# Optimization experiments

Measured on AMD Instinct MI355X. Metric: run time of the kernel, lower is better.

## Reference

```python
import jax, jax.numpy as jnp
import numpy as np
import math

D_MODEL = 1024
EXPAND = 2
D_INNER = EXPAND * D_MODEL        # 2048
HEADDIM = 64
NHEADS = D_INNER // HEADDIM       # 32
D_STATE = 128
D_CONV = 4
CHUNK = 128
SEQLEN = 4096
BATCH = 1                         # bidirectional merge in forward hard-codes batch=1
CONV_DIM = D_INNER + 2 * (2 * D_STATE)            # 2560
D_IN_PROJ = 2 * D_INNER + 2 * (2 * D_STATE) + 2 * NHEADS  # 4672
EPS = 1e-5


def silu(x):
    return x * jax.nn.sigmoid(x)


def segsum_exp(a):
    """exp(segsum(a)): out[..., i, j] = exp(sum_{k=j+1..i} a[..., k]) for i>=j else 0."""
    T = a.shape[-1]
    m1 = jnp.tril(jnp.ones((T, T), bool), -1)
    s = jnp.cumsum(jnp.where(m1, a[..., :, None], 0.0), axis=-2)
    m0 = jnp.tril(jnp.ones((T, T), bool))
    return jnp.where(m0, jnp.exp(jnp.where(m0, s, 0.0)), 0.0)


def ssd(x, A, B, C, chunk):
    """x:(b,L,h,p) A:(b,L,h) B,C:(b,L,n) (head dim of size 1 squeezed). L % chunk == 0."""
    b, L, h, p = x.shape
    c = L // chunk
    x = x.reshape(b, c, chunk, h, p)
    A = A.reshape(b, c, chunk, h).transpose(0, 3, 1, 2)   # (b,h,c,l)
    B = B.reshape(b, c, chunk, -1)
    C = C.reshape(b, c, chunk, -1)
    A_cs = jnp.cumsum(A, axis=-1)                          # (b,h,c,l)
    Lmat = segsum_exp(A)                                   # (b,h,c,l,l)
    # intra-chunk (diagonal block) outputs
    Y_diag = jnp.einsum('bcln,bcsn,bhcls,bcshp->bclhp', C, B, Lmat, x)
    # per-chunk states
    decay_states = jnp.exp(A_cs[..., -1:] - A_cs)          # (b,h,c,l)
    states = jnp.einsum('bcln,bhcl,bclhp->bchpn', B, decay_states, x)
    states = jnp.concatenate([jnp.zeros_like(states[:, :1]), states], axis=1)
    # inter-chunk recurrence via segsum over chunk boundaries
    decay_chunk = segsum_exp(jnp.pad(A_cs[..., -1], ((0, 0), (0, 0), (1, 0))))  # (b,h,c+1,c+1)
    new_states = jnp.einsum('bhzc,bchpn->bzhpn', decay_chunk, states)
    states, final_state = new_states[:, :-1], new_states[:, -1]
    Y_off = jnp.einsum('bcln,bchpn,bhcl->bclhp', C, states, jnp.exp(A_cs))
    Y = (Y_diag + Y_off).reshape(b, L, h, p)
    return Y, final_state


def setup_inputs() -> dict:
    key = jax.random.key(0)
    ks = jax.random.split(key, 8)
    s = 0.02
    u = jax.random.normal(ks[0], (BATCH, SEQLEN, D_MODEL), jnp.float32)
    in_proj_w = jax.random.normal(ks[1], (D_IN_PROJ, D_MODEL), jnp.float32) * s
    conv_w = jax.random.normal(ks[2], (CONV_DIM, 1, D_CONV), jnp.float32) * (1.0 / math.sqrt(D_CONV))
    conv_b = jnp.zeros((CONV_DIM,), jnp.float32)
    dt = jnp.exp(jax.random.uniform(ks[3], (NHEADS,)) * (math.log(0.1) - math.log(0.001)) + math.log(0.001))
    dt = jnp.clip(dt, 1e-4)
    dt_bias = dt + jnp.log(-jnp.expm1(-dt))
    A_log = jnp.log(jax.random.uniform(ks[4], (NHEADS,), minval=1.0, maxval=16.0))
    D = jnp.ones((NHEADS,), jnp.float32)
    fc_D_w = jax.random.normal(ks[5], (NHEADS, D_INNER), jnp.float32) * s
    norm_w = jnp.ones((D_INNER,), jnp.float32)
    out_proj_w = jax.random.normal(ks[6], (D_MODEL, D_INNER), jnp.float32) * s
    return dict(u=u, in_proj_w=in_proj_w, conv_w=conv_w, conv_b=conv_b, dt_bias=dt_bias,
                A_log=A_log, D=D, fc_D_w=fc_D_w, norm_w=norm_w, out_proj_w=out_proj_w)


def reference(u, in_proj_w, conv_w, conv_b, dt_bias, A_log, D, fc_D_w, norm_w, out_proj_w):
    b, l, _ = u.shape
    zxbcdt = u @ in_proj_w.T                               # (b,l,D_IN_PROJ)
    z = zxbcdt[..., :D_INNER]
    xBC = zxbcdt[..., D_INNER:D_INNER + CONV_DIM]
    dt = zxbcdt[..., D_INNER + CONV_DIM:]                  # (b,l,2*nheads)
    # fwd heads + time-reversed bwd heads stacked on batch dim
    dt = jnp.concatenate([dt[..., :NHEADS], jnp.flip(dt[..., NHEADS:], axis=1)], axis=0)
    dt = jax.nn.softplus(dt + dt_bias)                     # (2b,l,nheads)
    # depthwise causal conv1d + silu
    xc = jnp.transpose(xBC, (0, 2, 1))                     # (b,CONV_DIM,l)
    xc = jax.lax.conv_general_dilated(xc, conv_w, (1,), [(D_CONV - 1, 0)],
                                      feature_group_count=CONV_DIM,
                                      dimension_numbers=('NCH', 'OIH', 'NCH'))
    xc = xc + conv_b[None, :, None]
    xBC = silu(jnp.transpose(xc, (0, 2, 1)))               # (b,l,CONV_DIM)
    x = xBC[..., :D_INNER]
    BC = xBC[..., D_INNER:]
    x_og = x
    x2 = jnp.concatenate([x, jnp.flip(x, 1)], axis=0)      # (2b,l,d_inner)
    BC = jnp.concatenate([BC[..., :2 * D_STATE], jnp.flip(BC[..., 2 * D_STATE:], 1)], axis=0)
    B = BC[..., :D_STATE]
    C = BC[..., D_STATE:]
    xh = x2.reshape(2 * b, l, NHEADS, HEADDIM)
    A = -jnp.exp(A_log)
    Y, final_state = ssd(xh * dt[..., None], A * dt, B, C, CHUNK)
    y = Y + xh * D[:, None]
    y = y.reshape(2 * b, l, D_INNER)
    # torch.roll(shift=1, dim=1) then zero first step == shift right with zero pad
    y = jnp.concatenate([jnp.zeros_like(y[:, :1]), y[:, :-1]], axis=1)
    y_fw, y_bw = y[:b], jnp.flip(y[b:], 1)
    fd = x_og @ fc_D_w.T + D                               # F.linear(x_og, fc_D.weight, bias=D)
    y = y_fw + y_bw + x_og * jnp.repeat(fd, HEADDIM, axis=-1)
    # gated RMSNorm
    yg = y * silu(z)
    yn = yg * jax.lax.rsqrt(jnp.mean(yg * yg, axis=-1, keepdims=True) + EPS) * norm_w
    return yn @ out_proj_w.T
```

## Files before the change

### kernel.cpp

```cpp
#include <hip/hip_runtime.h>
#include <hip/hip_bf16.h>
#include <math.h>

#define L_SEQ   4096
#define DMODEL  1024
#define DINNER  2048
#define NHEADS  32
#define HEADDIM 64
#define DSTATE  128
#define NCHUNK  32
#define CHUNKL  128
#define CONVDIM 2560
#define DPROJ   4672
#define NPAD1   4736

typedef __hip_bfloat16 bf16;
__device__ __forceinline__ float b2f(bf16 x) { return __bfloat162float(x); }
__device__ __forceinline__ bf16 f2b(float x) { return __float2bfloat16(x); }
__device__ __forceinline__ float sh2f(short s) {
  return __uint_as_float(((unsigned int)(unsigned short)s) << 16);
}
__device__ __forceinline__ short f2bs(float x) {
  bf16 t = __float2bfloat16(x);
  return *reinterpret_cast<short*>(&t);
}

typedef __attribute__((ext_vector_type(8))) short bf16x8v;
typedef __attribute__((ext_vector_type(4))) float f32x4v;

__device__ __forceinline__ float dot8(bf16x8v x, float4 w0, float4 w1) {
  return sh2f(x[0]) * w0.x + sh2f(x[1]) * w0.y + sh2f(x[2]) * w0.z + sh2f(x[3]) * w0.w +
         sh2f(x[4]) * w1.x + sh2f(x[5]) * w1.y + sh2f(x[6]) * w1.z + sh2f(x[7]) * w1.w;
}


__global__ __launch_bounds__(256) void cast_kernel(
    const float* __restrict__ src, bf16* __restrict__ dst, int n_src, int n_tot) {
  int i = blockIdx.x * 256 + threadIdx.x;
  if (i < n_tot) dst[i] = (i < n_src) ? f2b(src[i]) : f2b(0.f);
}

template <typename TC>
__global__ __launch_bounds__(256) void gemm_mfma(
    const bf16* __restrict__ A, int lda,
    const bf16* __restrict__ B, int ldb,
    TC* __restrict__ C, int ldc,
    int N, int K, int gridM) {
  __shared__ short As[128][32];
  __shared__ short Bs[128][32];
  int tid = threadIdx.x;
  int lane = tid & 63;
  int w = tid >> 6;
  int wr = w >> 1, wc = w & 1;
  int bid = blockIdx.x;
  int mst = gridM >> 3;
  int xk = bid & 7, q = bid >> 3;
  int bm = (xk + 8 * (q % mst)) * 128;
  int bn = (q / mst) * 128;
  f32x4v acc[4][4];
#pragma unroll
  for (int i = 0; i < 4; i++)
#pragma unroll
    for (int j = 0; j < 4; j++) acc[i][j] = (f32x4v){0.f, 0.f, 0.f, 0.f};

  const bf16* Ab = A + (size_t)(bm + w * 32 + (lane >> 2)) * lda + (lane & 3) * 8;
  const bf16* Bb = B + (size_t)(bn + w * 32 + (lane >> 2)) * ldb + (lane & 3) * 8;

  for (int k0 = 0; k0 < K; k0 += 32) {
    __builtin_amdgcn_global_load_lds(
        (const __attribute__((address_space(1))) void*)(Ab + k0),
        (__attribute__((address_space(3))) void*)&As[w * 32][0], 16, 0, 0);
    __builtin_amdgcn_global_load_lds(
        (const __attribute__((address_space(1))) void*)(Ab + (size_t)16 * lda + k0),
        (__attribute__((address_space(3))) void*)&As[w * 32 + 16][0], 16, 0, 0);
    __builtin_amdgcn_global_load_lds(
        (const __attribute__((address_space(1))) void*)(Bb + k0),
        (__attribute__((address_space(3))) void*)&Bs[w * 32][0], 16, 0, 0);
    __builtin_amdgcn_global_load_lds(
        (const __attribute__((address_space(1))) void*)(Bb + (size_t)16 * ldb + k0),
        (__attribute__((address_space(3))) void*)&Bs[w * 32 + 16][0], 16, 0, 0);
    __syncthreads();
    bf16x8v af[4], bv[4];
#pragma unroll
    for (int i = 0; i < 4; i++)
      af[i] = *(const bf16x8v*)&As[wr * 64 + i * 16 + (lane & 15)][(lane >> 4) * 8];
#pragma unroll
    for (int j = 0; j < 4; j++)
      bv[j] = *(const bf16x8v*)&Bs[wc * 64 + j * 16 + (lane & 15)][(lane >> 4) * 8];
#pragma unroll
    for (int i = 0; i < 4; i++)
#pragma unroll
      for (int j = 0; j < 4; j++)
        acc[i][j] = __builtin_amdgcn_mfma_f32_16x16x32_bf16(af[i], bv[j], acc[i][j], 0, 0, 0);
    __syncthreads();
  }
  int quad = lane >> 4;
  int cn = lane & 15;
#pragma unroll
  for (int i = 0; i < 4; i++) {
#pragma unroll
    for (int j = 0; j < 4; j++) {
      int col = bn + wc * 64 + j * 16 + cn;
      if (col < N) {
#pragma unroll
        for (int r = 0; r < 4; r++) {
          int row = bm + wr * 64 + i * 16 + quad * 4 + r;
          float v = acc[i][j][r];
          if constexpr (sizeof(TC) == 2) C[(size_t)row * ldc + col] = f2b(v);
          else                           C[(size_t)row * ldc + col] = v;
        }
      }
    }
  }
}

__global__ __launch_bounds__(256) void fc_kernel(
    const bf16* __restrict__ xbc, const float* __restrict__ Wf,
    const float* __restrict__ Dp, float* __restrict__ fd) {
  int lane = threadIdx.x & 63;
  int w = threadIdx.x >> 6;
  int t0 = (blockIdx.x * 4 + w) * 4;
  int h = lane & 31;
  int g = lane >> 5;
  const float* wr = Wf + (size_t)h * DINNER + g * 1024;
  const bf16* xr = xbc + (size_t)t0 * CONVDIM + g * 1024;
  float a0 = 0.f, a1 = 0.f, a2 = 0.f, a3 = 0.f;
  for (int k = 0; k < 1024; k += 8) {
    float4 w0 = *(const float4*)(wr + k);
    float4 w1 = *(const float4*)(wr + k + 4);
    bf16x8v x0 = *(const bf16x8v*)(xr + k);
    bf16x8v x1 = *(const bf16x8v*)(xr + CONVDIM + k);
    bf16x8v x2 = *(const bf16x8v*)(xr + 2 * CONVDIM + k);
    bf16x8v x3 = *(const bf16x8v*)(xr + 3 * CONVDIM + k);
    a0 += dot8(x0, w0, w1);
    a1 += dot8(x1, w0, w1);
    a2 += dot8(x2, w0, w1);
    a3 += dot8(x3, w0, w1);
  }
  a0 += __shfl_down(a0, 32);
  a1 += __shfl_down(a1, 32);
  a2 += __shfl_down(a2, 32);
  a3 += __shfl_down(a3, 32);
  if (lane < 32) {
    float d = Dp[h];
    fd[(t0 + 0) * NHEADS + h] = a0 + d;
    fd[(t0 + 1) * NHEADS + h] = a1 + d;
    fd[(t0 + 2) * NHEADS + h] = a2 + d;
    fd[(t0 + 3) * NHEADS + h] = a3 + d;
  }
}

__global__ __launch_bounds__(256) void conv_silu_kernel(
    const bf16* __restrict__ zx, const float* __restrict__ conv_w,
    const float* __restrict__ conv_b, bf16* __restrict__ xbc) {
  int idx = blockIdx.x * 256 + threadIdx.x;
  if (idx >= (L_SEQ / 4) * CONVDIM) return;
  int ch = idx % CONVDIM;
  int t0 = (idx / CONVDIM) * 4;
  const bf16* col = zx + DINNER + ch;
  float w0 = conv_w[ch * 4 + 0], w1 = conv_w[ch * 4 + 1];
  float w2 = conv_w[ch * 4 + 2], w3 = conv_w[ch * 4 + 3];
  float bsv = conv_b[ch];
  float x[7];
#pragma unroll
  for (int i = 0; i < 7; i++) {
    int t = t0 - 3 + i;
    x[i] = (t >= 0) ? b2f(col[(size_t)t * DPROJ]) : 0.f;
  }
#pragma unroll
  for (int j = 0; j < 4; j++) {
    float acc = bsv + w0 * x[j] + w1 * x[j + 1] + w2 * x[j + 2] + w3 * x[j + 3];
    xbc[(size_t)(t0 + j) * CONVDIM + ch] = f2b(acc / (1.f + __expf(-acc)));
  }
}

__global__ __launch_bounds__(256) void dt_kernel(
    const bf16* __restrict__ zx, const float* __restrict__ dt_bias,
    float* __restrict__ dt2) {
  int idx = blockIdx.x * 256 + threadIdx.x;
  if (idx >= 2 * L_SEQ * NHEADS) return;
  int h = idx % NHEADS;
  int t = (idx / NHEADS) % L_SEQ;
  int b = idx / (NHEADS * L_SEQ);
  float v;
  if (b == 0) v = b2f(zx[(size_t)t * DPROJ + 4608 + h]);
  else        v = b2f(zx[(size_t)(L_SEQ - 1 - t) * DPROJ + 4608 + NHEADS + h]);
  v += dt_bias[h];
  dt2[idx] = (v > 20.f) ? v : log1pf(expf(v));
}

__global__ __launch_bounds__(256) void gmat_kernel(
    const bf16* __restrict__ xbc, bf16* __restrict__ G) {
  __shared__ bf16 Cs[128][136];
  __shared__ bf16 Bs[128][136];
  int bc = blockIdx.x;
  int b = bc / NCHUNK, c = bc % NCHUNK;
  int tid = threadIdx.x;
  int lane = tid & 63;
  int w = tid >> 6;
  int bofs = b ? 2304 : 2048;
  int cofs = b ? 2432 : 2176;
  for (int o = tid; o < CHUNKL * DSTATE / 8; o += 256) {
    int s = o >> 4;
    int n8 = (o & 15) * 8;
    int t = b ? (L_SEQ - 1 - (c * CHUNKL + s)) : (c * CHUNKL + s);
    const bf16* row = xbc + (size_t)t * CONVDIM;
    *(bf16x8v*)&Bs[s][n8] = *(const bf16x8v*)&row[bofs + n8];
    *(bf16x8v*)&Cs[s][n8] = *(const bf16x8v*)&row[cofs + n8];
  }
  __syncthreads();
  f32x4v acc[2][8];
#pragma unroll
  for (int i = 0; i < 2; i++)
#pragma unroll
    for (int j = 0; j < 8; j++) acc[i][j] = (f32x4v){0.f, 0.f, 0.f, 0.f};
#pragma unroll
  for (int k0 = 0; k0 < 128; k0 += 32) {
    bf16x8v a0 = *(const bf16x8v*)&Cs[w * 32 + (lane & 15)][(lane >> 4) * 8 + k0];
    bf16x8v a1 = *(const bf16x8v*)&Cs[w * 32 + 16 + (lane & 15)][(lane >> 4) * 8 + k0];
#pragma unroll
    for (int j = 0; j < 8; j++) {
      bf16x8v bv = *(const bf16x8v*)&Bs[j * 16 + (lane & 15)][(lane >> 4) * 8 + k0];
      acc[0][j] = __builtin_amdgcn_mfma_f32_16x16x32_bf16(a0, bv, acc[0][j], 0, 0, 0);
      acc[1][j] = __builtin_amdgcn_mfma_f32_16x16x32_bf16(a1, bv, acc[1][j], 0, 0, 0);
    }
  }
  int quad = lane >> 4, cn = lane & 15;
  bf16* Gb = G + (size_t)bc * CHUNKL * CHUNKL;
#pragma unroll
  for (int i = 0; i < 2; i++)
#pragma unroll
    for (int j = 0; j < 8; j++)
#pragma unroll
      for (int r = 0; r < 4; r++) {
        int l = w * 32 + i * 16 + quad * 4 + r;
        int s = j * 16 + cn;
        Gb[l * CHUNKL + s] = f2b(acc[i][j][r]);
      }
}

__global__ __launch_bounds__(256) void chunk_kernel(
    const bf16* __restrict__ xbc, const float* __restrict__ dt2,
    const float* __restrict__ A_log,
    bf16* __restrict__ states, float* __restrict__ csum) {
  int gid = blockIdx.x;
  int h = gid % NHEADS;
  int bc = gid / NHEADS;
  int c = bc % NCHUNK, b = bc / NCHUNK;
  int tid = threadIdx.x;
  int lane = tid & 63;
  int w = tid >> 6;
  __shared__ bf16 BdT[128][136];
  __shared__ bf16 xdtT[64][136];
  __shared__ float acs[CHUNKL];
  __shared__ float dtl[CHUNKL];
  __shared__ float decays[CHUNKL];
  if (tid < CHUNKL)
    dtl[tid] = dt2[((size_t)b * L_SEQ + c * CHUNKL + tid) * NHEADS + h];
  __syncthreads();
  if (tid == 0) {
    float Ah = -__expf(A_log[h]);
    float s = 0.f;
    for (int l = 0; l < CHUNKL; l++) { s += Ah * dtl[l]; acs[l] = s; }
    csum[gid] = __expf(s);
  }
  __syncthreads();
  if (tid < CHUNKL) decays[tid] = __expf(acs[CHUNKL - 1] - acs[tid]);
  for (int o = tid; o < CHUNKL * HEADDIM / 8; o += 256) {
    int s = o & 127;
    int p8 = (o >> 7) * 8;
    int t = b ? (L_SEQ - 1 - (c * CHUNKL + s)) : (c * CHUNKL + s);
    bf16x8v xv = *(const bf16x8v*)&xbc[(size_t)t * CONVDIM + h * HEADDIM + p8];
    float d = dtl[s];
#pragma unroll
    for (int j = 0; j < 8; j++) xdtT[p8 + j][s] = f2b(sh2f(xv[j]) * d);
  }
  __syncthreads();
  for (int o = tid; o < CHUNKL * CHUNKL / 8; o += 256) {
    int l = o & 127;
    int n8 = (o >> 7) * 8;
    int t = b ? (L_SEQ - 1 - (c * CHUNKL + l)) : (c * CHUNKL + l);
    bf16x8v bv = *(const bf16x8v*)&xbc[(size_t)t * CONVDIM + (b ? 2304 : 2048) + n8];
    float d = decays[l];
#pragma unroll
    for (int j = 0; j < 8; j++) BdT[n8 + j][l] = f2b(sh2f(bv[j]) * d);
  }
  __syncthreads();
  f32x4v accS[8];
#pragma unroll
  for (int j = 0; j < 8; j++) accS[j] = (f32x4v){0.f, 0.f, 0.f, 0.f};
#pragma unroll
  for (int k0 = 0; k0 < 128; k0 += 32) {
    bf16x8v av = *(const bf16x8v*)&xdtT[w * 16 + (lane & 15)][(lane >> 4) * 8 + k0];
#pragma unroll
    for (int j = 0; j < 8; j++) {
      bf16x8v bv = *(const bf16x8v*)&BdT[j * 16 + (lane & 15)][(lane >> 4) * 8 + k0];
      accS[j] = __builtin_amdgcn_mfma_f32_16x16x32_bf16(av, bv, accS[j], 0, 0, 0);
    }
  }
  int quad = lane >> 4, cn = lane & 15;
  bf16* st = states + (size_t)gid * (HEADDIM * DSTATE);
#pragma unroll
  for (int j = 0; j < 8; j++)
#pragma unroll
    for (int r = 0; r < 4; r++) {
      int p = w * 16 + quad * 4 + r;
      int n = j * 16 + cn;
      st[p * DSTATE + n] = f2b(accS[j][r]);
    }
}

__global__ __launch_bounds__(256) void scan_kernel(
    bf16* __restrict__ states, const float* __restrict__ csum) {
  int idx = blockIdx.x * 256 + threadIdx.x;
  int n = idx % DSTATE;
  int p = (idx / DSTATE) % HEADDIM;
  int h = (idx / (DSTATE * HEADDIM)) % NHEADS;
  int b = idx / (DSTATE * HEADDIM * NHEADS);
  float S = 0.f;
  for (int c = 0; c < NCHUNK; c++) {
    int gid = (b * NCHUNK + c) * NHEADS + h;
    size_t off = (size_t)gid * (HEADDIM * DSTATE) + p * DSTATE + n;
    float tmp = b2f(states[off]);
    states[off] = f2b(S);
    S = csum[gid] * S + tmp;
  }
}

__global__ __launch_bounds__(256) void yoff_kernel(
    const bf16* __restrict__ xbc, const float* __restrict__ dt2,
    const float* __restrict__ A_log, const bf16* __restrict__ G,
    const bf16* __restrict__ states, const float* __restrict__ Dp,
    bf16* __restrict__ Y) {
  int gid = blockIdx.x;
  int h = gid % NHEADS;
  int bc = gid / NHEADS;
  int c = bc % NCHUNK, b = bc / NCHUNK;
  int tid = threadIdx.x;
  int lane = tid & 63;
  int w = tid >> 6;
  __shared__ bf16 WB[128][136];
  __shared__ bf16 SX[64][136];
  __shared__ float acs[CHUNKL];
  __shared__ float dtl[CHUNKL];
  __shared__ float eAl[CHUNKL];
  if (tid < CHUNKL)
    dtl[tid] = dt2[((size_t)b * L_SEQ + c * CHUNKL + tid) * NHEADS + h];
  __syncthreads();
  if (tid == 0) {
    float Ah = -__expf(A_log[h]);
    float s = 0.f;
    for (int l = 0; l < CHUNKL; l++) { s += Ah * dtl[l]; acs[l] = s; }
  }
  __syncthreads();
  if (tid < CHUNKL) eAl[tid] = __expf(acs[tid]);
  for (int o = tid; o < CHUNKL * HEADDIM / 8; o += 256) {
    int s = o & 127;
    int p8 = (o >> 7) * 8;
    int t = b ? (L_SEQ - 1 - (c * CHUNKL + s)) : (c * CHUNKL + s);
    bf16x8v xv = *(const bf16x8v*)&xbc[(size_t)t * CONVDIM + h * HEADDIM + p8];
    float d = dtl[s];
#pragma unroll
    for (int j = 0; j < 8; j++) SX[p8 + j][s] = f2b(sh2f(xv[j]) * d);
  }
  {
    const bf16* Gb = G + (size_t)bc * CHUNKL * CHUNKL;
    for (int o = tid; o < CHUNKL * CHUNKL / 8; o += 256) {
      int l = o >> 4;
      int s8 = (o & 15) * 8;
      bf16x8v g = *(const bf16x8v*)&Gb[l * CHUNKL + s8];
      float al = acs[l];
      bf16x8v wv;
#pragma unroll
      for (int j = 0; j < 8; j++) {
        int s = s8 + j;
        float e = (s <= l) ? sh2f(g[j]) * __expf(al - acs[s]) : 0.f;
        wv[j] = f2bs(e);
      }
      *(bf16x8v*)&WB[l][s8] = wv;
    }
  }
  __syncthreads();
  f32x4v accY[2][4];
#pragma unroll
  for (int i = 0; i < 2; i++)
#pragma unroll
    for (int j = 0; j < 4; j++) accY[i][j] = (f32x4v){0.f, 0.f, 0.f, 0.f};
#pragma unroll
  for (int k0 = 0; k0 < 128; k0 += 32) {
    bf16x8v a0 = *(const bf16x8v*)&WB[w * 32 + (lane & 15)][(lane >> 4) * 8 + k0];
    bf16x8v a1 = *(const bf16x8v*)&WB[w * 32 + 16 + (lane & 15)][(lane >> 4) * 8 + k0];
#pragma unroll
    for (int j = 0; j < 4; j++) {
      bf16x8v bv = *(const bf16x8v*)&SX[j * 16 + (lane & 15)][(lane >> 4) * 8 + k0];
      accY[0][j] = __builtin_amdgcn_mfma_f32_16x16x32_bf16(a0, bv, accY[0][j], 0, 0, 0);
      accY[1][j] = __builtin_amdgcn_mfma_f32_16x16x32_bf16(a1, bv, accY[1][j], 0, 0, 0);
    }
  }
  __syncthreads();
  {
    int cofs = b ? 2432 : 2176;
    for (int o = tid; o < CHUNKL * DSTATE / 8; o += 256) {
      int l = o >> 4;
      int n8 = (o & 15) * 8;
      int t = b ? (L_SEQ - 1 - (c * CHUNKL + l)) : (c * CHUNKL + l);
      bf16x8v cv = *(const bf16x8v*)&xbc[(size_t)t * CONVDIM + cofs + n8];
      float e = eAl[l];
      bf16x8v ov;
#pragma unroll
      for (int j = 0; j < 8; j++) ov[j] = f2bs(sh2f(cv[j]) * e);
      *(bf16x8v*)&WB[l][n8] = ov;
    }
    const bf16* stp = states + (size_t)gid * (HEADDIM * DSTATE);
    for (int o = tid; o < HEADDIM * DSTATE / 8; o += 256) {
      int p = o >> 4;
      int n8 = (o & 15) * 8;
      *(bf16x8v*)&SX[p][n8] = *(const bf16x8v*)&stp[o * 8];
    }
  }
  __syncthreads();
#pragma unroll
  for (int k0 = 0; k0 < 128; k0 += 32) {
    bf16x8v a0 = *(const bf16x8v*)&WB[w * 32 + (lane & 15)][(lane >> 4) * 8 + k0];
    bf16x8v a1 = *(const bf16x8v*)&WB[w * 32 + 16 + (lane & 15)][(lane >> 4) * 8 + k0];
#pragma unroll
    for (int j = 0; j < 4; j++) {
      bf16x8v bv = *(const bf16x8v*)&SX[j * 16 + (lane & 15)][(lane >> 4) * 8 + k0];
      accY[0][j] = __builtin_amdgcn_mfma_f32_16x16x32_bf16(a0, bv, accY[0][j], 0, 0, 0);
      accY[1][j] = __builtin_amdgcn_mfma_f32_16x16x32_bf16(a1, bv, accY[1][j], 0, 0, 0);
    }
  }
  int quad = lane >> 4, cn = lane & 15;
  float Dh = Dp[h];
#pragma unroll
  for (int i = 0; i < 2; i++)
#pragma unroll
    for (int j = 0; j < 4; j++)
#pragma unroll
      for (int r = 0; r < 4; r++) {
        int l = w * 32 + i * 16 + quad * 4 + r;
        int p = j * 16 + cn;
        int t = b ? (L_SEQ - 1 - (c * CHUNKL + l)) : (c * CHUNKL + l);
        float xv = b2f(xbc[(size_t)t * CONVDIM + h * HEADDIM + p]);
        size_t yi = ((size_t)b * L_SEQ + c * CHUNKL + l) * DINNER + h * HEADDIM + p;
        Y[yi] = f2b(accY[i][j][r] + xv * Dh);
      }
}

__global__ __launch_bounds__(256) void combine_kernel(
    const bf16* __restrict__ Y, const bf16* __restrict__ xbc,
    const bf16* __restrict__ zx, const float* __restrict__ fd,
    const float* __restrict__ norm_w, bf16* __restrict__ yn) {
  int t = blockIdx.x;
  int tid = threadIdx.x;
  int j8 = tid * 8;
  float yf[8], yb[8];
#pragma unroll
  for (int j = 0; j < 8; j++) { yf[j] = 0.f; yb[j] = 0.f; }
  if (t >= 1) {
    bf16x8v v = *(const bf16x8v*)&Y[(size_t)(t - 1) * DINNER + j8];
#pragma unroll
    for (int j = 0; j < 8; j++) yf[j] = sh2f(v[j]);
  }
  if (t <= L_SEQ - 2) {
    bf16x8v v = *(const bf16x8v*)&Y[((size_t)L_SEQ + (L_SEQ - 2 - t)) * DINNER + j8];
#pragma unroll
    for (int j = 0; j < 8; j++) yb[j] = sh2f(v[j]);
  }
  bf16x8v xogv = *(const bf16x8v*)&xbc[(size_t)t * CONVDIM + j8];
  bf16x8v zv = *(const bf16x8v*)&zx[(size_t)t * DPROJ + j8];
  float fdv = fd[t * NHEADS + (j8 >> 6)];
  float yg[8];
  float ss = 0.f;
#pragma unroll
  for (int j = 0; j < 8; j++) {
    float y = yf[j] + yb[j] + sh2f(xogv[j]) * fdv;
    float z = sh2f(zv[j]);
    float g = y * (z / (1.f + __expf(-z)));
    yg[j] = g;
    ss += g * g;
  }
#pragma unroll
  for (int off = 32; off > 0; off >>= 1) ss += __shfl_down(ss, off);
  __shared__ float red[4];
  if ((tid & 63) == 0) red[tid >> 6] = ss;
  __syncthreads();
  float tot = red[0] + red[1] + red[2] + red[3];
  float scale = rsqrtf(tot / (float)DINNER + 1e-5f);
  float4 nw0 = *(const float4*)&norm_w[j8];
  float4 nw1 = *(const float4*)&norm_w[j8 + 4];
  bf16x8v ov;
  ov[0] = f2bs(yg[0] * scale * nw0.x);
  ov[1] = f2bs(yg[1] * scale * nw0.y);
  ov[2] = f2bs(yg[2] * scale * nw0.z);
  ov[3] = f2bs(yg[3] * scale * nw0.w);
  ov[4] = f2bs(yg[4] * scale * nw1.x);
  ov[5] = f2bs(yg[5] * scale * nw1.y);
  ov[6] = f2bs(yg[6] * scale * nw1.z);
  ov[7] = f2bs(yg[7] * scale * nw1.w);
  *(bf16x8v*)&yn[(size_t)t * DINNER + j8] = ov;
}

extern "C" void kernel_launch(void* const* d_in, const int* in_sizes, int n_in,
                              void* d_out, int out_size, void* d_ws, size_t ws_size,
                              hipStream_t stream) {
  const float* u         = (const float*)d_in[0];
  const float* in_proj_w = (const float*)d_in[1];
  const float* conv_w    = (const float*)d_in[2];
  const float* conv_b    = (const float*)d_in[3];
  const float* dt_bias   = (const float*)d_in[4];
  const float* A_log     = (const float*)d_in[5];
  const float* Dp        = (const float*)d_in[6];
  const float* fc_D_w    = (const float*)d_in[7];
  const float* norm_w    = (const float*)d_in[8];
  const float* out_proj_w= (const float*)d_in[9];
  float* out = (float*)d_out;

  char* base = (char*)d_ws;
  bf16*  zx  = (bf16*)base;  base += (size_t)L_SEQ * DPROJ * 2;
  bf16*  xbc = (bf16*)base;  base += (size_t)L_SEQ * CONVDIM * 2;
  float* dt2 = (float*)base; base += (size_t)2 * L_SEQ * NHEADS * 4;
  bf16*  G   = (bf16*)base;  base += (size_t)2 * NCHUNK * CHUNKL * CHUNKL * 4;
  bf16*  Yb  = (bf16*)base;  base += (size_t)2 * L_SEQ * DINNER * 4;
  bf16*  stb = (bf16*)base;  base += (size_t)2 * NCHUNK * NHEADS * HEADDIM * DSTATE * 4;
  float* cs  = (float*)base; base += (size_t)2 * NCHUNK * NHEADS * 4;
  bf16*  u_bf   = (bf16*)Yb;
  bf16*  w1p_bf = (bf16*)((char*)Yb + 9437184);
  bf16*  w2_bf  = (bf16*)G;
  bf16*  yn     = (bf16*)stb;
  float* fd     = (float*)((char*)stb + 33554432);

  cast_kernel<<<(L_SEQ * DMODEL + 255) / 256, 256, 0, stream>>>(
      u, u_bf, L_SEQ * DMODEL, L_SEQ * DMODEL);
  cast_kernel<<<(NPAD1 * DMODEL + 255) / 256, 256, 0, stream>>>(
      in_proj_w, w1p_bf, DPROJ * DMODEL, NPAD1 * DMODEL);
  gemm_mfma<bf16><<<(L_SEQ / 128) * (NPAD1 / 128), 256, 0, stream>>>(
      u_bf, DMODEL, w1p_bf, DMODEL, zx, DPROJ, DPROJ, DMODEL, L_SEQ / 128);
  conv_silu_kernel<<<((L_SEQ / 4) * CONVDIM + 255) / 256, 256, 0, stream>>>(
      zx, conv_w, conv_b, xbc);
  dt_kernel<<<(2 * L_SEQ * NHEADS + 255) / 256, 256, 0, stream>>>(
      zx, dt_bias, dt2);
  gmat_kernel<<<2 * NCHUNK, 256, 0, stream>>>(xbc, G);
  chunk_kernel<<<2 * NCHUNK * NHEADS, 256, 0, stream>>>(
      xbc, dt2, A_log, stb, cs);
  scan_kernel<<<(2 * NHEADS * HEADDIM * DSTATE) / 256, 256, 0, stream>>>(stb, cs);
  yoff_kernel<<<2 * NCHUNK * NHEADS, 256, 0, stream>>>(
      xbc, dt2, A_log, G, stb, Dp, Yb);
  cast_kernel<<<(DMODEL * DINNER + 255) / 256, 256, 0, stream>>>(
      out_proj_w, w2_bf, DMODEL * DINNER, DMODEL * DINNER);
  fc_kernel<<<L_SEQ / 16, 256, 0, stream>>>(xbc, fc_D_w, Dp, fd);
  combine_kernel<<<L_SEQ, 256, 0, stream>>>(Yb, xbc, zx, fd, norm_w, yn);
  gemm_mfma<float><<<(L_SEQ / 128) * (DMODEL / 128), 256, 0, stream>>>(
      yn, DINNER, w2_bf, DINNER, out, DMODEL, DMODEL, DINNER, L_SEQ / 128);
}
```

Baseline: 413.5 us.

## Merge cast and conv/dt launches, split gmat into quarters, preload scan chunks

Merges the two input casts into one launch and the conv/SiLU and dt kernels into one launch, which removes launch overhead. Splits gmat into four blocks per chunk so it runs on 256 blocks instead of 64, and each block computes only the lower-triangular tiles its warp needs. The scan kernel now loads all chunk states and decay factors up front, so the loads no longer sit on the serial dependency chain. The first GEMM drops its block swizzle for row-major block order, which may change L2 reuse.

```diff
diff --git a/kernel.cpp b/kernel.cpp
--- a/kernel.cpp
+++ b/kernel.cpp
@@ -34,6 +34,20 @@
 }
 
 
+__global__ __launch_bounds__(256) void cast2_kernel(
+    const float* __restrict__ u, const float* __restrict__ w1,
+    bf16* __restrict__ u_bf, bf16* __restrict__ w1_bf) {
+  const int NU = (L_SEQ * DMODEL) / 256;
+  int bid = blockIdx.x;
+  if (bid < NU) {
+    int i = bid * 256 + threadIdx.x;
+    u_bf[i] = f2b(u[i]);
+  } else {
+    int i = (bid - NU) * 256 + threadIdx.x;
+    w1_bf[i] = (i < DPROJ * DMODEL) ? f2b(w1[i]) : f2b(0.f);
+  }
+}
+
 __global__ __launch_bounds__(256) void cast_kernel(
     const float* __restrict__ src, bf16* __restrict__ dst, int n_src, int n_tot) {
   int i = blockIdx.x * 256 + threadIdx.x;
@@ -45,7 +59,7 @@
     const bf16* __restrict__ A, int lda,
     const bf16* __restrict__ B, int ldb,
     TC* __restrict__ C, int ldc,
-    int N, int K, int gridM) {
+    int N, int K, int gridM, int gridN, int swz) {
   __shared__ short As[128][32];
   __shared__ short Bs[128][32];
   int tid = threadIdx.x;
@@ -53,10 +67,16 @@
   int w = tid >> 6;
   int wr = w >> 1, wc = w & 1;
   int bid = blockIdx.x;
-  int mst = gridM >> 3;
-  int xk = bid & 7, q = bid >> 3;
-  int bm = (xk + 8 * (q % mst)) * 128;
-  int bn = (q / mst) * 128;
+  int bm, bn;
+  if (swz) {
+    int mst = gridM >> 3;
+    int xk = bid & 7, q = bid >> 3;
+    bm = (xk + 8 * (q % mst)) * 128;
+    bn = (q / mst) * 128;
+  } else {
+    bm = (bid / gridN) * 128;
+    bn = (bid % gridN) * 128;
+  }
   f32x4v acc[4][4];
 #pragma unroll
   for (int i = 0; i < 4; i++)
@@ -150,51 +170,53 @@
   }
 }
 
-__global__ __launch_bounds__(256) void conv_silu_kernel(
+#define CONV_BLOCKS ((L_SEQ / 4) * CONVDIM / 256)
+__global__ __launch_bounds__(256) void conv_dt_kernel(
     const bf16* __restrict__ zx, const float* __restrict__ conv_w,
-    const float* __restrict__ conv_b, bf16* __restrict__ xbc) {
-  int idx = blockIdx.x * 256 + threadIdx.x;
-  if (idx >= (L_SEQ / 4) * CONVDIM) return;
-  int ch = idx % CONVDIM;
-  int t0 = (idx / CONVDIM) * 4;
-  const bf16* col = zx + DINNER + ch;
-  float w0 = conv_w[ch * 4 + 0], w1 = conv_w[ch * 4 + 1];
-  float w2 = conv_w[ch * 4 + 2], w3 = conv_w[ch * 4 + 3];
-  float bsv = conv_b[ch];
-  float x[7];
-#pragma unroll
-  for (int i = 0; i < 7; i++) {
-    int t = t0 - 3 + i;
-    x[i] = (t >= 0) ? b2f(col[(size_t)t * DPROJ]) : 0.f;
-  }
-#pragma unroll
-  for (int j = 0; j < 4; j++) {
-    float acc = bsv + w0 * x[j] + w1 * x[j + 1] + w2 * x[j + 2] + w3 * x[j + 3];
-    xbc[(size_t)(t0 + j) * CONVDIM + ch] = f2b(acc / (1.f + __expf(-acc)));
-  }
-}
-
-__global__ __launch_bounds__(256) void dt_kernel(
-    const bf16* __restrict__ zx, const float* __restrict__ dt_bias,
-    float* __restrict__ dt2) {
-  int idx = blockIdx.x * 256 + threadIdx.x;
-  if (idx >= 2 * L_SEQ * NHEADS) return;
-  int h = idx % NHEADS;
-  int t = (idx / NHEADS) % L_SEQ;
-  int b = idx / (NHEADS * L_SEQ);
-  float v;
-  if (b == 0) v = b2f(zx[(size_t)t * DPROJ + 4608 + h]);
-  else        v = b2f(zx[(size_t)(L_SEQ - 1 - t) * DPROJ + 4608 + NHEADS + h]);
-  v += dt_bias[h];
-  dt2[idx] = (v > 20.f) ? v : log1pf(expf(v));
+    const float* __restrict__ conv_b, bf16* __restrict__ xbc,
+    const float* __restrict__ dt_bias, float* __restrict__ dt2) {
+  int bid = blockIdx.x;
+  if (bid < CONV_BLOCKS) {
+    int idx = bid * 256 + threadIdx.x;
+    int ch = idx % CONVDIM;
+    int t0 = (idx / CONVDIM) * 4;
+    const bf16* col = zx + DINNER + ch;
+    float w0 = conv_w[ch * 4 + 0], w1 = conv_w[ch * 4 + 1];
+    float w2 = conv_w[ch * 4 + 2], w3 = conv_w[ch * 4 + 3];
+    float bsv = conv_b[ch];
+    float x[7];
+#pragma unroll
+    for (int i = 0; i < 7; i++) {
+      int t = t0 - 3 + i;
+      x[i] = (t >= 0) ? b2f(col[(size_t)t * DPROJ]) : 0.f;
+    }
+#pragma unroll
+    for (int j = 0; j < 4; j++) {
+      float acc = bsv + w0 * x[j] + w1 * x[j + 1] + w2 * x[j + 2] + w3 * x[j + 3];
+      xbc[(size_t)(t0 + j) * CONVDIM + ch] = f2b(acc / (1.f + __expf(-acc)));
+    }
+  } else {
+    int idx = (bid - CONV_BLOCKS) * 256 + threadIdx.x;
+    int h = idx % NHEADS;
+    int t = (idx / NHEADS) % L_SEQ;
+    int b = idx / (NHEADS * L_SEQ);
+    float v;
+    if (b == 0) v = b2f(zx[(size_t)t * DPROJ + 4608 + h]);
+    else        v = b2f(zx[(size_t)(L_SEQ - 1 - t) * DPROJ + 4608 + NHEADS + h]);
+    v += dt_bias[h];
+    dt2[idx] = (v > 20.f) ? v : log1pf(expf(v));
+  }
 }
 
 __global__ __launch_bounds__(256) void gmat_kernel(
     const bf16* __restrict__ xbc, bf16* __restrict__ G) {
-  __shared__ bf16 Cs[128][136];
+  __shared__ bf16 Cs[32][136];
   __shared__ bf16 Bs[128][136];
-  int bc = blockIdx.x;
+  int blk = blockIdx.x;
+  int quarter = blk & 3;
+  int bc = blk >> 2;
   int b = bc / NCHUNK, c = bc % NCHUNK;
+  int l0 = quarter * 32;
   int tid = threadIdx.x;
   int lane = tid & 63;
   int w = tid >> 6;
@@ -204,23 +226,28 @@
     int s = o >> 4;
     int n8 = (o & 15) * 8;
     int t = b ? (L_SEQ - 1 - (c * CHUNKL + s)) : (c * CHUNKL + s);
-    const bf16* row = xbc + (size_t)t * CONVDIM;
-    *(bf16x8v*)&Bs[s][n8] = *(const bf16x8v*)&row[bofs + n8];
-    *(bf16x8v*)&Cs[s][n8] = *(const bf16x8v*)&row[cofs + n8];
-  }
-  __syncthreads();
-  f32x4v acc[2][8];
+    *(bf16x8v*)&Bs[s][n8] = *(const bf16x8v*)&xbc[(size_t)t * CONVDIM + bofs + n8];
+  }
+  for (int o = tid; o < 32 * DSTATE / 8; o += 256) {
+    int l = o >> 4;
+    int n8 = (o & 15) * 8;
+    int t = b ? (L_SEQ - 1 - (c * CHUNKL + l0 + l)) : (c * CHUNKL + l0 + l);
+    *(bf16x8v*)&Cs[l][n8] = *(const bf16x8v*)&xbc[(size_t)t * CONVDIM + cofs + n8];
+  }
+  __syncthreads();
+  if (w > quarter) return;
+  f32x4v acc[2][2];
 #pragma unroll
   for (int i = 0; i < 2; i++)
 #pragma unroll
-    for (int j = 0; j < 8; j++) acc[i][j] = (f32x4v){0.f, 0.f, 0.f, 0.f};
+    for (int j = 0; j < 2; j++) acc[i][j] = (f32x4v){0.f, 0.f, 0.f, 0.f};
 #pragma unroll
   for (int k0 = 0; k0 < 128; k0 += 32) {
-    bf16x8v a0 = *(const bf16x8v*)&Cs[w * 32 + (lane & 15)][(lane >> 4) * 8 + k0];
-    bf16x8v a1 = *(const bf16x8v*)&Cs[w * 32 + 16 + (lane & 15)][(lane >> 4) * 8 + k0];
-#pragma unroll
-    for (int j = 0; j < 8; j++) {
-      bf16x8v bv = *(const bf16x8v*)&Bs[j * 16 + (lane & 15)][(lane >> 4) * 8 + k0];
+    bf16x8v a0 = *(const bf16x8v*)&Cs[(lane & 15)][(lane >> 4) * 8 + k0];
+    bf16x8v a1 = *(const bf16x8v*)&Cs[16 + (lane & 15)][(lane >> 4) * 8 + k0];
+#pragma unroll
+    for (int j = 0; j < 2; j++) {
+      bf16x8v bv = *(const bf16x8v*)&Bs[(2 * w + j) * 16 + (lane & 15)][(lane >> 4) * 8 + k0];
       acc[0][j] = __builtin_amdgcn_mfma_f32_16x16x32_bf16(a0, bv, acc[0][j], 0, 0, 0);
       acc[1][j] = __builtin_amdgcn_mfma_f32_16x16x32_bf16(a1, bv, acc[1][j], 0, 0, 0);
     }
@@ -230,11 +257,11 @@
 #pragma unroll
   for (int i = 0; i < 2; i++)
 #pragma unroll
-    for (int j = 0; j < 8; j++)
+    for (int j = 0; j < 2; j++)
 #pragma unroll
       for (int r = 0; r < 4; r++) {
-        int l = w * 32 + i * 16 + quad * 4 + r;
-        int s = j * 16 + cn;
+        int l = l0 + i * 16 + quad * 4 + r;
+        int s = (2 * w + j) * 16 + cn;
         Gb[l * CHUNKL + s] = f2b(acc[i][j][r]);
       }
 }
@@ -317,13 +344,18 @@
   int p = (idx / DSTATE) % HEADDIM;
   int h = (idx / (DSTATE * HEADDIM)) % NHEADS;
   int b = idx / (DSTATE * HEADDIM * NHEADS);
+  size_t base = ((size_t)(b * NCHUNK) * NHEADS + h) * (HEADDIM * DSTATE) + p * DSTATE + n;
+  const size_t cstride = (size_t)NHEADS * HEADDIM * DSTATE;
+  float tmp[NCHUNK], cv[NCHUNK];
+#pragma unroll
+  for (int c = 0; c < NCHUNK; c++) tmp[c] = b2f(states[base + c * cstride]);
+#pragma unroll
+  for (int c = 0; c < NCHUNK; c++) cv[c] = csum[(b * NCHUNK + c) * NHEADS + h];
   float S = 0.f;
+#pragma unroll
   for (int c = 0; c < NCHUNK; c++) {
-    int gid = (b * NCHUNK + c) * NHEADS + h;
-    size_t off = (size_t)gid * (HEADDIM * DSTATE) + p * DSTATE + n;
-    float tmp = b2f(states[off]);
-    states[off] = f2b(S);
-    S = csum[gid] * S + tmp;
+    states[base + c * cstride] = f2b(S);
+    S = cv[c] * S + tmp[c];
   }
 }
 
@@ -530,17 +562,14 @@
   bf16*  yn     = (bf16*)stb;
   float* fd     = (float*)((char*)stb + 33554432);
 
-  cast_kernel<<<(L_SEQ * DMODEL + 255) / 256, 256, 0, stream>>>(
-      u, u_bf, L_SEQ * DMODEL, L_SEQ * DMODEL);
-  cast_kernel<<<(NPAD1 * DMODEL + 255) / 256, 256, 0, stream>>>(
-      in_proj_w, w1p_bf, DPROJ * DMODEL, NPAD1 * DMODEL);
+  cast2_kernel<<<(L_SEQ * DMODEL + NPAD1 * DMODEL) / 256, 256, 0, stream>>>(
+      u, in_proj_w, u_bf, w1p_bf);
   gemm_mfma<bf16><<<(L_SEQ / 128) * (NPAD1 / 128), 256, 0, stream>>>(
-      u_bf, DMODEL, w1p_bf, DMODEL, zx, DPROJ, DPROJ, DMODEL, L_SEQ / 128);
-  conv_silu_kernel<<<((L_SEQ / 4) * CONVDIM + 255) / 256, 256, 0, stream>>>(
-      zx, conv_w, conv_b, xbc);
-  dt_kernel<<<(2 * L_SEQ * NHEADS + 255) / 256, 256, 0, stream>>>(
-      zx, dt_bias, dt2);
-  gmat_kernel<<<2 * NCHUNK, 256, 0, stream>>>(xbc, G);
+      u_bf, DMODEL, w1p_bf, DMODEL, zx, DPROJ, DPROJ, DMODEL,
+      L_SEQ / 128, NPAD1 / 128, 0);
+  conv_dt_kernel<<<CONV_BLOCKS + (2 * L_SEQ * NHEADS) / 256, 256, 0, stream>>>(
+      zx, conv_w, conv_b, xbc, dt_bias, dt2);
+  gmat_kernel<<<2 * NCHUNK * 4, 256, 0, stream>>>(xbc, G);
   chunk_kernel<<<2 * NCHUNK * NHEADS, 256, 0, stream>>>(
       xbc, dt2, A_log, stb, cs);
   scan_kernel<<<(2 * NHEADS * HEADDIM * DSTATE) / 256, 256, 0, stream>>>(stb, cs);
@@ -551,5 +580,6 @@
   fc_kernel<<<L_SEQ / 16, 256, 0, stream>>>(xbc, fc_D_w, Dp, fd);
   combine_kernel<<<L_SEQ, 256, 0, stream>>>(Yb, xbc, zx, fd, norm_w, yn);
   gemm_mfma<float><<<(L_SEQ / 128) * (DMODEL / 128), 256, 0, stream>>>(
-      yn, DINNER, w2_bf, DINNER, out, DMODEL, DMODEL, DINNER, L_SEQ / 128);
-}
+      yn, DINNER, w2_bf, DINNER, out, DMODEL, DMODEL, DINNER,
+      L_SEQ / 128, DMODEL / 128, 1);
+}
```

Result: no change. 411.9 us (-0.4%).
